# Optimization experiments

Hardware: AMD Instinct MI355X
Metric: run time of the kernel (lower is better)

Reference implementation:

```python
import jax, jax.numpy as jnp
import numpy as np

B, S, IN, H, NH = 64, 512, 512, 1024, 4
HD = H // NH
A, HID = 18, 1024
EPS = 1e-5


def _ln(x, w, eps=EPS):
    mu = jnp.mean(x, axis=-1, keepdims=True)
    var = jnp.mean((x - mu) ** 2, axis=-1, keepdims=True)
    return (x - mu) * jax.lax.rsqrt(var + eps) * w


def setup_inputs() -> dict:
    key = jax.random.key(0)
    ks = jax.random.split(key, 12)
    g = lambda k, shape, s: jax.random.normal(k, shape, jnp.float32) * s
    return {
        "obs": g(ks[0], (B, S, IN), 1.0),
        "slstm_state": jnp.zeros((4, B, H), jnp.float32),  # (y, c, n, m)
        "W_in": g(ks[1], (H, IN), IN ** -0.5),
        "b_in": jnp.zeros((H,), jnp.float32),
        "ln1_w": jnp.ones((H,), jnp.float32),
        "w_gates": g(ks[2], (4, NH, HD, HD), HD ** -0.5),  # i,f,z,o headwise input proj
        "R": g(ks[3], (NH, HD, 4, HD), HD ** -0.5),        # headwise recurrent kernel
        "b_gates": jnp.zeros((4, H), jnp.float32),
        "gn_w": jnp.ones((H,), jnp.float32),               # multi-head group norm weight
        "ln_post_w": jnp.ones((H,), jnp.float32),          # post-blocks norm
        "W_hid": g(ks[4], (HID, H), H ** -0.5), "b_hid": jnp.zeros((HID,), jnp.float32),
        "W_pol": g(ks[5], (HID, HID), HID ** -0.5), "b_pol": jnp.zeros((HID,), jnp.float32),
        "W_val": g(ks[6], (HID, HID), HID ** -0.5), "b_val": jnp.zeros((HID,), jnp.float32),
        "W_act": g(ks[7], (A, HID), 0.01), "b_act": jnp.zeros((A,), jnp.float32),
        "W_v": g(ks[8], (1, HID), HID ** -0.5), "b_v": jnp.zeros((1,), jnp.float32),
    }


def reference(obs, slstm_state, W_in, b_in, ln1_w, w_gates, R, b_gates, gn_w,
              ln_post_w, W_hid, b_hid, W_pol, b_pol, W_val, b_val, W_act, b_act, W_v, b_v):
    b, s, _ = obs.shape
    # input projection (input_size != hidden_size -> nn.Linear)
    x_proj = obs @ W_in.T + b_in                      # (B,S,H)
    # sLSTM block pre-norm
    xn = _ln(x_proj, ln1_w)
    xh = xn.reshape(b, s, NH, HD)
    # headwise (block-diagonal) gate input preactivations, time-major for scan
    gx = jnp.einsum('bsnd,gnde->sgbne', xh, w_gates)  # (S,4,B,NH,HD)
    bg = b_gates.reshape(4, 1, NH, HD)
    st = slstm_state.reshape(4, b, NH, HD)

    def step(carry, gx_t):
        h, c, n, m = carry
        raw = gx_t + jnp.einsum('bnd,ndge->gbne', h, R) + bg  # (4,B,NH,HD)
        iraw, fraw, zraw, oraw = raw
        logfplusm = m + jax.nn.log_sigmoid(fraw)
        mnew = jnp.maximum(iraw, logfplusm)
        i = jnp.exp(iraw - mnew)
        f = jnp.exp(logfplusm - mnew)
        cnew = f * c + i * jnp.tanh(zraw)
        nnew = f * n + i
        hnew = jax.nn.sigmoid(oraw) * cnew / nnew
        return (hnew, cnew, nnew, mnew), hnew

    _, ys = jax.lax.scan(step, (st[0], st[1], st[2], st[3]), gx)  # (S,B,NH,HD)
    y = jnp.transpose(ys, (1, 0, 2, 3))               # (B,S,NH,HD)
    # multi-head group norm over head_dim, then residual
    mu = jnp.mean(y, axis=-1, keepdims=True)
    var = jnp.mean((y - mu) ** 2, axis=-1, keepdims=True)
    y_gn = (y - mu) * jax.lax.rsqrt(var + EPS) * gn_w.reshape(NH, HD)
    out = x_proj + y_gn.reshape(b, s, H)
    out = _ln(out, ln_post_w)                         # post_blocks_norm
    # actor-critic heads
    hh = jax.nn.relu(out @ W_hid.T + b_hid)
    hp = jax.nn.relu(hh @ W_pol.T + b_pol)
    hv = jax.nn.relu(hh @ W_val.T + b_val)
    logits = hp @ W_act.T + b_act                     # (B,S,A)
    value = hv @ W_v.T + b_v                          # (B,S,1)
    return logits, value
```

## Files before the change

kernel.cpp:

```cpp
#include <hip/hip_runtime.h>
#include <cstdint>
#include <cstddef>

#define B_ 64
#define S_ 512
#define IN_ 512
#define H_ 1024
#define NH_ 4
#define HD_ 256
#define A_ 18
#define HID_ 1024
#define TCH_ 128
#define NCH_ (S_ / TCH_)

using short8 = __attribute__((ext_vector_type(8))) short;
using f32x4  = __attribute__((ext_vector_type(4))) float;

__device__ __forceinline__ unsigned short f2bf(float f) {
  union { float f; unsigned u; } c; c.f = f;
  unsigned r = c.u + 0x7FFFu + ((c.u >> 16) & 1u);
  return (unsigned short)(r >> 16);
}
__device__ __forceinline__ float bf2f(unsigned short h) {
  union { unsigned u; float f; } c; c.u = ((unsigned)h) << 16;
  return c.f;
}
__device__ __forceinline__ unsigned pk2(float a, float b) {
  return (unsigned)f2bf(a) | ((unsigned)f2bf(b) << 16);
}
__device__ __forceinline__ float dot2(unsigned a, unsigned b, float c) {
  float d;
  asm("v_dot2_f32_bf16 %0, %1, %2, %3" : "=v"(d) : "v"(a), "v"(b), "v"(c));
  return d;
}

__global__ __launch_bounds__(256) void rtrans_k(const float* __restrict__ R,
                                                unsigned* __restrict__ Rbb,
                                                unsigned* __restrict__ Rl) {
  const int i = blockIdx.x * 256 + threadIdx.x;
  const int dp = i & 127;
  const int e = (i >> 7) & 255;
  const int g = (i >> 15) & 3;
  const int nh = i >> 17;
  const float* rp = R + (((size_t)nh * 256 + 2 * dp) * 4 + g) * 256 + e;
  unsigned lo = f2bf(rp[0]), hi = f2bf(rp[1024]);
  unsigned v = lo | (hi << 16);
  Rbb[i] = v;
  if (dp >= 96) {
    int j = (dp - 96) >> 1, p = (dp - 96) & 1;
    int col = g * 256 + e;
    Rl[((size_t)(j * 4 + nh) * 1024 + col) * 2 + p] = v;
  }
}

__global__ __launch_bounds__(256) void wgt_k(const float* __restrict__ wg,
                                             unsigned short* __restrict__ wgb) {
  const int i = blockIdx.x * 256 + threadIdx.x;
  const int k = i & 255;
  const int e = (i >> 8) & 255;
  const int g = (i >> 16) & 3;
  const int nh = i >> 18;
  wgb[i] = f2bf(wg[(((size_t)(g * 4 + nh) * 256 + k) * 256) + e]);
}

__global__ __launch_bounds__(256) void wbf_k(const float* __restrict__ src,
                                             unsigned short* __restrict__ dst, int n) {
  int i = blockIdx.x * 256 + threadIdx.x;
  if (i < n) dst[i] = f2bf(src[i]);
}

__global__ __launch_bounds__(256) void rowstats_k(const unsigned short* __restrict__ x,
                                                  float* __restrict__ rs) {
  const int r = blockIdx.x, tid = threadIdx.x;
  const int lane = tid & 63, wave = tid >> 6;
  ushort4 u = *(const ushort4*)(x + (size_t)r * H_ + tid * 4);
  float v0 = bf2f(u.x), v1 = bf2f(u.y), v2 = bf2f(u.z), v3 = bf2f(u.w);
  float s1 = v0 + v1 + v2 + v3;
  float s2 = v0 * v0 + v1 * v1 + v2 * v2 + v3 * v3;
#pragma unroll
  for (int off = 32; off; off >>= 1) { s1 += __shfl_xor(s1, off); s2 += __shfl_xor(s2, off); }
  __shared__ float a1[4], a2[4];
  if (lane == 0) { a1[wave] = s1; a2[wave] = s2; }
  __syncthreads();
  if (tid == 0) {
    float S1 = a1[0] + a1[1] + a1[2] + a1[3];
    float S2 = a2[0] + a2[1] + a2[2] + a2[3];
    float mu = S1 * (1.f / H_);
    float var = S2 * (1.f / H_) - mu * mu;
    rs[r * 2] = mu;
    rs[r * 2 + 1] = rsqrtf(var + 1e-5f);
  }
}

template <int AMODE, int BMODE, bool RELU, int OUTMODE>
__global__ __launch_bounds__(256) void mgemm_k(
    const void* __restrict__ Av, const void* __restrict__ Wv,
    const float* __restrict__ bias, const float* __restrict__ rs,
    const float* __restrict__ lnw, unsigned short* __restrict__ Cb,
    int K, int lda, int chunk) {
  __shared__ uint4 As4[4][128];
  __shared__ uint4 Bs4[4][128];
  const int tid = threadIdx.x;
  const int lane = tid & 63, wave = tid >> 6;
  const int wr = wave >> 1, wc = wave & 1;
  const int col0 = blockIdx.y * 128;
  int nh = 0, g = 0, aoff = 0, bb = 0;
  size_t wbase = 0;
  if constexpr (OUTMODE == 1) {
    int z = blockIdx.z; nh = z >> 2; g = z & 3;
    aoff = nh * HD_;
    bb = blockIdx.x;
    wbase = (size_t)(nh * 4 + g) * 256 * 256;
  }
  auto arow = [&](int mm) -> int {
    if constexpr (OUTMODE == 1) return bb * 512 + chunk * TCH_ + mm;
    else return (int)blockIdx.x * 128 + mm;
  };
  f32x4 acc[4][4];
#pragma unroll
  for (int m = 0; m < 4; ++m)
#pragma unroll
    for (int n = 0; n < 4; ++n) acc[m][n] = 0.f;

  const int sm = tid >> 1;
  const int sh = tid & 1;

  for (int k0 = 0; k0 < K; k0 += 32) {
    {
      int rg = arow(sm);
      unsigned pk[8];
      if constexpr (AMODE == 0) {
        const float* ap = (const float*)Av + (size_t)rg * lda + k0 + sh * 16;
#pragma unroll
        for (int q = 0; q < 4; ++q) {
          float4 f = ((const float4*)ap)[q];
          pk[2 * q] = pk2(f.x, f.y); pk[2 * q + 1] = pk2(f.z, f.w);
        }
      } else if constexpr (AMODE == 1) {
        const uint4* ap = (const uint4*)((const unsigned short*)Av + (size_t)rg * lda + aoff + k0 + sh * 16);
        uint4 u0 = ap[0], u1 = ap[1];
        pk[0] = u0.x; pk[1] = u0.y; pk[2] = u0.z; pk[3] = u0.w;
        pk[4] = u1.x; pk[5] = u1.y; pk[6] = u1.z; pk[7] = u1.w;
      } else {
        const uint4* ap = (const uint4*)((const unsigned short*)Av + (size_t)rg * lda + aoff + k0 + sh * 16);
        uint4 u0 = ap[0], u1 = ap[1];
        unsigned w8[8] = {u0.x, u0.y, u0.z, u0.w, u1.x, u1.y, u1.z, u1.w};
        float mu = rs[rg * 2], rstd = rs[rg * 2 + 1];
        const float* lw = lnw + aoff + k0 + sh * 16;
#pragma unroll
        for (int q = 0; q < 8; ++q) {
          float lo = (bf2f((unsigned short)w8[q]) - mu) * rstd * lw[2 * q];
          float hi = (bf2f((unsigned short)(w8[q] >> 16)) - mu) * rstd * lw[2 * q + 1];
          pk[q] = pk2(lo, hi);
        }
      }
      As4[2 * sh][sm]     = uint4{pk[0], pk[1], pk[2], pk[3]};
      As4[2 * sh + 1][sm] = uint4{pk[4], pk[5], pk[6], pk[7]};
    }
    {
      unsigned pk[8];
      if constexpr (BMODE == 0) {
        const float* wp = (const float*)Wv + (size_t)(col0 + sm) * K + k0 + sh * 16;
#pragma unroll
        for (int q = 0; q < 4; ++q) {
          float4 f = ((const float4*)wp)[q];
          pk[2 * q] = pk2(f.x, f.y); pk[2 * q + 1] = pk2(f.z, f.w);
        }
      } else if constexpr (BMODE == 1) {
        const uint4* wp = (const uint4*)((const unsigned short*)Wv + wbase + (size_t)(col0 + sm) * 256 + k0 + sh * 16);
        uint4 u0 = wp[0], u1 = wp[1];
        pk[0] = u0.x; pk[1] = u0.y; pk[2] = u0.z; pk[3] = u0.w;
        pk[4] = u1.x; pk[5] = u1.y; pk[6] = u1.z; pk[7] = u1.w;
      } else {
        const uint4* wp = (const uint4*)((const unsigned short*)Wv + (size_t)(col0 + sm) * K + k0 + sh * 16);
        uint4 u0 = wp[0], u1 = wp[1];
        pk[0] = u0.x; pk[1] = u0.y; pk[2] = u0.z; pk[3] = u0.w;
        pk[4] = u1.x; pk[5] = u1.y; pk[6] = u1.z; pk[7] = u1.w;
      }
      Bs4[2 * sh][sm]     = uint4{pk[0], pk[1], pk[2], pk[3]};
      Bs4[2 * sh + 1][sm] = uint4{pk[4], pk[5], pk[6], pk[7]};
    }
    __syncthreads();
    short8 af[4], bfv[4];
#pragma unroll
    for (int m = 0; m < 4; ++m)
      af[m] = *(const short8*)&As4[lane >> 4][wr * 64 + m * 16 + (lane & 15)];
#pragma unroll
    for (int n = 0; n < 4; ++n)
      bfv[n] = *(const short8*)&Bs4[lane >> 4][wc * 64 + n * 16 + (lane & 15)];
#pragma unroll
    for (int m = 0; m < 4; ++m)
#pragma unroll
      for (int n = 0; n < 4; ++n)
        acc[m][n] = __builtin_amdgcn_mfma_f32_16x16x32_bf16(af[m], bfv[n], acc[m][n], 0, 0, 0);
    __syncthreads();
  }
  if constexpr (OUTMODE == 0) {
#pragma unroll
    for (int n = 0; n < 4; ++n) {
      int c = col0 + wc * 64 + n * 16 + (lane & 15);
      float bc = bias ? bias[c] : 0.f;
#pragma unroll
      for (int m = 0; m < 4; ++m) {
        int r0 = arow(wr * 64 + m * 16 + ((lane >> 4) << 2));
#pragma unroll
        for (int i = 0; i < 4; ++i) {
          float v = acc[m][n][i] + bc;
          if constexpr (RELU) v = fmaxf(v, 0.f);
          Cb[(size_t)(r0 + i) * 1024 + c] = f2bf(v);
        }
      }
    }
  } else {
#pragma unroll
    for (int n = 0; n < 4; ++n) {
      int e = col0 + wc * 64 + n * 16 + (lane & 15);
#pragma unroll
      for (int m = 0; m < 4; ++m) {
        int sl0 = wr * 64 + m * 16 + ((lane >> 4) << 2);
#pragma unroll
        for (int i = 0; i < 4; ++i) {
          int sl = sl0 + i;
          size_t base = (size_t)(sl * 64 + bb) * 4096 + nh * 1024 + g * 256;
          Cb[base + e] = f2bf(acc[m][n][i]);
        }
      }
    }
  }
}

__global__ __launch_bounds__(512, 2) void scan_k(
    const unsigned short* __restrict__ gxc, const unsigned* __restrict__ Rbb,
    const unsigned* __restrict__ Rl, const float* __restrict__ bgates,
    float* __restrict__ state, unsigned short* __restrict__ y, int chunk) {
  const int tid = threadIdx.x;
  const int bid = blockIdx.x;
  const int nh = bid >> 6, b = bid & 63;
  const int col0 = tid, col1 = tid + 512;
  const int g0 = col0 >> 8, g1 = col1 >> 8;
  __shared__ uint2 Rlds[16][1024];
  __shared__ float rawf[1024];
  __shared__ alignas(16) unsigned short hsu[256];

#pragma unroll
  for (int it = 0; it < 32; ++it) {
    int idx = it * 512 + tid;
    int j = idx >> 10, col = idx & 1023;
    Rlds[j][col] = ((const uint2*)Rl)[(size_t)(j * 4 + nh) * 1024 + col];
  }
  unsigned rc0[96], rc1[96];
  {
    const unsigned* rp0 = Rbb + ((size_t)nh * 1024 + col0) * 128;
    const unsigned* rp1 = Rbb + ((size_t)nh * 1024 + col1) * 128;
#pragma unroll
    for (int i = 0; i < 96; ++i) rc0[i] = rp0[i];
#pragma unroll
    for (int i = 0; i < 96; ++i) rc1[i] = rp1[i];
  }
  const float bg0 = bgates[g0 * H_ + nh * HD_ + (col0 & 255)];
  const float bg1 = bgates[g1 * H_ + nh * HD_ + (col1 & 255)];

  const size_t sbase = (size_t)b * H_ + nh * HD_ + tid;
  float c_ = 0.f, n_ = 0.f, m_ = 0.f, hlast = 0.f;
  if (tid < 256) {
    hlast = state[sbase];
    c_ = state[65536 + sbase];
    n_ = state[2 * 65536 + sbase];
    m_ = state[3 * 65536 + sbase];
    hsu[tid] = f2bf(hlast);
  }
  __syncthreads();

  const unsigned short* gp0 = gxc + ((size_t)b * 4 + nh) * 1024 + col0;
  const unsigned short* gp1 = gp0 + 512;
  unsigned short* yp = y + ((size_t)(chunk * TCH_) * 64 + b) * H_ + nh * HD_;

  unsigned short gc0 = gp0[0], gc1 = gp1[0];

  for (int t = 0; t < TCH_; ++t) {
    float acc0 = bf2f(gc0) + bg0;
    float acc1 = bf2f(gc1) + bg1;
    if (t < TCH_ - 1) {
      gc0 = gp0[(size_t)(t + 1) * 262144];
      gc1 = gp1[(size_t)(t + 1) * 262144];
    }
    const uint4* h4 = (const uint4*)hsu;
#pragma unroll
    for (int q = 0; q < 24; ++q) {
      uint4 hu = h4[q];
      acc0 = dot2(rc0[4 * q + 0], hu.x, acc0);
      acc1 = dot2(rc1[4 * q + 0], hu.x, acc1);
      acc0 = dot2(rc0[4 * q + 1], hu.y, acc0);
      acc1 = dot2(rc1[4 * q + 1], hu.y, acc1);
      acc0 = dot2(rc0[4 * q + 2], hu.z, acc0);
      acc1 = dot2(rc1[4 * q + 2], hu.z, acc1);
      acc0 = dot2(rc0[4 * q + 3], hu.w, acc0);
      acc1 = dot2(rc1[4 * q + 3], hu.w, acc1);
    }
#pragma unroll
    for (int s = 0; s < 8; ++s) {
      uint4 hu = h4[24 + s];
      uint2 a0 = Rlds[2 * s][col0];
      uint2 a1 = Rlds[2 * s + 1][col0];
      uint2 b0 = Rlds[2 * s][col1];
      uint2 b1 = Rlds[2 * s + 1][col1];
      acc0 = dot2(a0.x, hu.x, acc0);
      acc1 = dot2(b0.x, hu.x, acc1);
      acc0 = dot2(a0.y, hu.y, acc0);
      acc1 = dot2(b0.y, hu.y, acc1);
      acc0 = dot2(a1.x, hu.z, acc0);
      acc1 = dot2(b1.x, hu.z, acc1);
      acc0 = dot2(a1.y, hu.w, acc0);
      acc1 = dot2(b1.y, hu.w, acc1);
    }
    float val0, val1;
    if (g0 == 0) {
      val0 = acc0;
    } else {
      float ls = -log1pf(expf(-fabsf(acc0)));
      if (acc0 < 0.f) ls += acc0;
      val0 = ls;
    }
    if (g1 == 2) {
      val1 = tanhf(acc1);
    } else {
      val1 = 1.f / (1.f + expf(-acc1));
    }
    rawf[col0] = val0;
    rawf[col1] = val1;
    __syncthreads();
    if (tid < 256) {
      float iraw = rawf[tid];
      float ls   = rawf[256 + tid];
      float tz   = rawf[512 + tid];
      float sg   = rawf[768 + tid];
      float lfm = m_ + ls;
      float mnew = fmaxf(iraw, lfm);
      float iv = expf(iraw - mnew);
      float fv = expf(lfm - mnew);
      c_ = fv * c_ + iv * tz;
      n_ = fv * n_ + iv;
      m_ = mnew;
      hlast = sg * c_ / n_;
      unsigned short hb = f2bf(hlast);
      hsu[tid] = hb;
      yp[(size_t)t * 65536 + tid] = hb;
    }
    __syncthreads();
  }
  if (tid < 256) {
    state[sbase] = hlast;
    state[65536 + sbase] = c_;
    state[2 * 65536 + sbase] = n_;
    state[3 * 65536 + sbase] = m_;
  }
}

__global__ __launch_bounds__(256) void post_k(
    const unsigned short* __restrict__ y, const unsigned short* __restrict__ xp,
    const float* __restrict__ gnw, const float* __restrict__ lpw,
    unsigned short* __restrict__ outb) {
  const int r = blockIdx.x;
  const int b = r >> 9, s = r & 511;
  const int tid = threadIdx.x;
  const int lane = tid & 63, wave = tid >> 6;
  ushort4 yu = *(const ushort4*)(y + (size_t)(s * 64 + b) * H_ + tid * 4);
  float v[4] = {bf2f(yu.x), bf2f(yu.y), bf2f(yu.z), bf2f(yu.w)};
  float s1 = v[0] + v[1] + v[2] + v[3];
  float s2 = v[0] * v[0] + v[1] * v[1] + v[2] * v[2] + v[3] * v[3];
#pragma unroll
  for (int off = 32; off; off >>= 1) { s1 += __shfl_xor(s1, off); s2 += __shfl_xor(s2, off); }
  float mu = s1 * (1.f / HD_);
  float rstd = rsqrtf(s2 * (1.f / HD_) - mu * mu + 1e-5f);
  float4 g4 = *(const float4*)(gnw + tid * 4);
  ushort4 xu = *(const ushort4*)(xp + (size_t)r * H_ + tid * 4);
  float o[4];
  o[0] = fmaf((v[0] - mu) * rstd, g4.x, bf2f(xu.x));
  o[1] = fmaf((v[1] - mu) * rstd, g4.y, bf2f(xu.y));
  o[2] = fmaf((v[2] - mu) * rstd, g4.z, bf2f(xu.z));
  o[3] = fmaf((v[3] - mu) * rstd, g4.w, bf2f(xu.w));
  float t1 = o[0] + o[1] + o[2] + o[3];
  float t2 = o[0] * o[0] + o[1] * o[1] + o[2] * o[2] + o[3] * o[3];
#pragma unroll
  for (int off = 32; off; off >>= 1) { t1 += __shfl_xor(t1, off); t2 += __shfl_xor(t2, off); }
  __shared__ float a1[4], a2[4];
  if (lane == 0) { a1[wave] = t1; a2[wave] = t2; }
  __syncthreads();
  float T1 = a1[0] + a1[1] + a1[2] + a1[3];
  float T2 = a2[0] + a2[1] + a2[2] + a2[3];
  float MU = T1 * (1.f / H_);
  float RS = rsqrtf(T2 * (1.f / H_) - MU * MU + 1e-5f);
  float4 w4 = *(const float4*)(lpw + tid * 4);
  ushort4 res = {f2bf((o[0] - MU) * RS * w4.x), f2bf((o[1] - MU) * RS * w4.y),
                 f2bf((o[2] - MU) * RS * w4.z), f2bf((o[3] - MU) * RS * w4.w)};
  *(ushort4*)(outb + (size_t)r * H_ + tid * 4) = res;
}

__global__ __launch_bounds__(256) void heads_k(
    const unsigned short* __restrict__ hp, const unsigned short* __restrict__ hv,
    const float* __restrict__ Wact, const float* __restrict__ bact,
    const float* __restrict__ Wv, const float* __restrict__ bv,
    float* __restrict__ dout) {
  const int lane = threadIdx.x & 63, wave = threadIdx.x >> 6;
  const int r = blockIdx.x * 4 + wave;
  const unsigned short* hpr = hp + (size_t)r * HID_;
  const unsigned short* hvr = hv + (size_t)r * HID_;
  float acc[A_];
#pragma unroll
  for (int j = 0; j < A_; ++j) acc[j] = 0.f;
  float accv = 0.f;
  for (int i = 0; i < 16; ++i) {
    int k = i * 64 + lane;
    float hpv = bf2f(hpr[k]);
    float hvv = bf2f(hvr[k]);
#pragma unroll
    for (int j = 0; j < A_; ++j) acc[j] = fmaf(hpv, Wact[j * HID_ + k], acc[j]);
    accv = fmaf(hvv, Wv[k], accv);
  }
#pragma unroll
  for (int j = 0; j < A_; ++j)
#pragma unroll
    for (int off = 32; off; off >>= 1) acc[j] += __shfl_xor(acc[j], off);
#pragma unroll
  for (int off = 32; off; off >>= 1) accv += __shfl_xor(accv, off);
  if (lane == 0) {
#pragma unroll
    for (int j = 0; j < A_; ++j) dout[(size_t)r * A_ + j] = acc[j] + bact[j];
    dout[589824 + r] = accv + bv[0];
  }
}

extern "C" void kernel_launch(void* const* d_in, const int* in_sizes, int n_in,
                              void* d_out, int out_size, void* d_ws, size_t ws_size,
                              hipStream_t stream) {
  const float* obs   = (const float*)d_in[0];
  const float* st    = (const float*)d_in[1];
  const float* W_in  = (const float*)d_in[2];
  const float* b_in  = (const float*)d_in[3];
  const float* ln1w  = (const float*)d_in[4];
  const float* wg    = (const float*)d_in[5];
  const float* R     = (const float*)d_in[6];
  const float* bgat  = (const float*)d_in[7];
  const float* gnw   = (const float*)d_in[8];
  const float* lpw   = (const float*)d_in[9];
  const float* W_hid = (const float*)d_in[10];
  const float* b_hid = (const float*)d_in[11];
  const float* W_pol = (const float*)d_in[12];
  const float* b_pol = (const float*)d_in[13];
  const float* W_val = (const float*)d_in[14];
  const float* b_val = (const float*)d_in[15];
  const float* W_act = (const float*)d_in[16];
  const float* b_act = (const float*)d_in[17];
  const float* W_v   = (const float*)d_in[18];
  const float* b_v   = (const float*)d_in[19];

  const size_t NEEDED = 214958080;
  if (ws_size < NEEDED) return;
  char* ws = (char*)d_ws;
  unsigned short* xproj = (unsigned short*)(ws + 0);
  unsigned short* gxc   = (unsigned short*)(ws + 67108864);
  unsigned short* ybuf  = (unsigned short*)(ws + 134217728);
  float* statebuf       = (float*)(ws + 201326592);
  float* rstat          = (float*)(ws + 202375168);
  unsigned* Rbb         = (unsigned*)(ws + 202899456);
  unsigned short* wgb   = (unsigned short*)(ws + 204996608);
  unsigned* Rl          = (unsigned*)(ws + 207093760);
  unsigned short* wib   = (unsigned short*)(ws + 207618048);
  unsigned short* whb   = (unsigned short*)(ws + 208666624);
  unsigned short* wpb   = (unsigned short*)(ws + 210763776);
  unsigned short* wvb   = (unsigned short*)(ws + 212860928);
  unsigned short* outb  = gxc;
  unsigned short* hh    = xproj;
  unsigned short* hp    = ybuf;
  unsigned short* hv    = gxc;
  float* dout = (float*)d_out;

  hipMemcpyAsync(statebuf, st, 4 * 65536 * sizeof(float), hipMemcpyDeviceToDevice, stream);
  rtrans_k<<<2048, 256, 0, stream>>>(R, Rbb, Rl);
  wgt_k<<<4096, 256, 0, stream>>>(wg, wgb);
  wbf_k<<<2048, 256, 0, stream>>>(W_in, wib, 524288);
  wbf_k<<<4096, 256, 0, stream>>>(W_hid, whb, 1048576);
  wbf_k<<<4096, 256, 0, stream>>>(W_pol, wpb, 1048576);
  wbf_k<<<4096, 256, 0, stream>>>(W_val, wvb, 1048576);
  mgemm_k<0, 2, false, 0><<<dim3(256, 8), 256, 0, stream>>>(
      obs, wib, b_in, nullptr, nullptr, xproj, 512, 512, 0);
  rowstats_k<<<32768, 256, 0, stream>>>(xproj, rstat);
  for (int c = 0; c < NCH_; ++c) {
    mgemm_k<2, 1, false, 1><<<dim3(64, 2, 16), 256, 0, stream>>>(
        xproj, wgb, nullptr, rstat, ln1w, gxc, 256, 1024, c);
    scan_k<<<256, 512, 0, stream>>>(gxc, Rbb, Rl, bgat, statebuf, ybuf, c);
  }
  post_k<<<32768, 256, 0, stream>>>(ybuf, xproj, gnw, lpw, outb);
  mgemm_k<1, 2, true, 0><<<dim3(256, 8), 256, 0, stream>>>(
      outb, whb, b_hid, nullptr, nullptr, hh, 1024, 1024, 0);
  mgemm_k<1, 2, true, 0><<<dim3(256, 8), 256, 0, stream>>>(
      hh, wpb, b_pol, nullptr, nullptr, hp, 1024, 1024, 0);
  mgemm_k<1, 2, true, 0><<<dim3(256, 8), 256, 0, stream>>>(
      hh, wvb, b_val, nullptr, nullptr, hv, 1024, 1024, 0);
  heads_k<<<8192, 256, 0, stream>>>(hp, hv, W_act, b_act, W_v, b_v, dout);
}
```

Baseline: 2.067 ms.

## Broadcast recurrent state via readlane SGPRs and widen LDS R-tile loads

In the recurrent scan, each lane now loads one 16-byte slice of the hidden state, and the values are broadcast with readlane into scalar registers that feed v_dot2 directly. This replaces the per-iteration LDS broadcast reads of h. The LDS-resident part of R is relaid out (and the prep kernel rewritten to match) so each column reads one uint4 per step instead of two uint2. Each column's dot product is split into two accumulators to shorten the dependency chain. The cost is extra readlane instructions and a slight change in floating-point summation order.

Measured after the change: 2.012 ms. 2.7% less time.

```diff
diff --git a/kernel.cpp b/kernel.cpp
--- a/kernel.cpp
+++ b/kernel.cpp
@@ -28,9 +28,9 @@
 __device__ __forceinline__ unsigned pk2(float a, float b) {
   return (unsigned)f2bf(a) | ((unsigned)f2bf(b) << 16);
 }
-__device__ __forceinline__ float dot2(unsigned a, unsigned b, float c) {
+__device__ __forceinline__ float dot2s(unsigned r, unsigned h_sgpr, float c) {
   float d;
-  asm("v_dot2_f32_bf16 %0, %1, %2, %3" : "=v"(d) : "v"(a), "v"(b), "v"(c));
+  asm("v_dot2_f32_bf16 %0, %1, %2, %3" : "=v"(d) : "v"(r), "s"(h_sgpr), "v"(c));
   return d;
 }
 
@@ -47,9 +47,9 @@
   unsigned v = lo | (hi << 16);
   Rbb[i] = v;
   if (dp >= 96) {
-    int j = (dp - 96) >> 1, p = (dp - 96) & 1;
+    int s = (dp - 96) >> 2, j = (dp - 96) & 3;
     int col = g * 256 + e;
-    Rl[((size_t)(j * 4 + nh) * 1024 + col) * 2 + p] = v;
+    Rl[((size_t)(nh * 1024 + col) * 8 + s) * 4 + j] = v;
   }
 }
 
@@ -234,19 +234,19 @@
     const unsigned* __restrict__ Rl, const float* __restrict__ bgates,
     float* __restrict__ state, unsigned short* __restrict__ y, int chunk) {
   const int tid = threadIdx.x;
+  const int lane = tid & 63;
   const int bid = blockIdx.x;
   const int nh = bid >> 6, b = bid & 63;
   const int col0 = tid, col1 = tid + 512;
   const int g0 = col0 >> 8, g1 = col1 >> 8;
-  __shared__ uint2 Rlds[16][1024];
+  __shared__ uint4 Rlds4[8][1024];
   __shared__ float rawf[1024];
   __shared__ alignas(16) unsigned short hsu[256];
 
 #pragma unroll
-  for (int it = 0; it < 32; ++it) {
+  for (int it = 0; it < 16; ++it) {
     int idx = it * 512 + tid;
-    int j = idx >> 10, col = idx & 1023;
-    Rlds[j][col] = ((const uint2*)Rl)[(size_t)(j * 4 + nh) * 1024 + col];
+    Rlds4[idx & 7][idx >> 3] = ((const uint4*)Rl)[(size_t)nh * 8192 + idx];
   }
   unsigned rc0[96], rc1[96];
   {
@@ -278,41 +278,48 @@
   unsigned short gc0 = gp0[0], gc1 = gp1[0];
 
   for (int t = 0; t < TCH_; ++t) {
-    float acc0 = bf2f(gc0) + bg0;
-    float acc1 = bf2f(gc1) + bg1;
+    float a0a = bf2f(gc0) + bg0, a0b = 0.f;
+    float a1a = bf2f(gc1) + bg1, a1b = 0.f;
     if (t < TCH_ - 1) {
       gc0 = gp0[(size_t)(t + 1) * 262144];
       gc1 = gp1[(size_t)(t + 1) * 262144];
     }
-    const uint4* h4 = (const uint4*)hsu;
+    uint4 hc = ((const uint4*)hsu)[lane & 31];
 #pragma unroll
     for (int q = 0; q < 24; ++q) {
-      uint4 hu = h4[q];
-      acc0 = dot2(rc0[4 * q + 0], hu.x, acc0);
-      acc1 = dot2(rc1[4 * q + 0], hu.x, acc1);
-      acc0 = dot2(rc0[4 * q + 1], hu.y, acc0);
-      acc1 = dot2(rc1[4 * q + 1], hu.y, acc1);
-      acc0 = dot2(rc0[4 * q + 2], hu.z, acc0);
-      acc1 = dot2(rc1[4 * q + 2], hu.z, acc1);
-      acc0 = dot2(rc0[4 * q + 3], hu.w, acc0);
-      acc1 = dot2(rc1[4 * q + 3], hu.w, acc1);
+      unsigned h0 = __builtin_amdgcn_readlane(hc.x, q);
+      unsigned h1 = __builtin_amdgcn_readlane(hc.y, q);
+      unsigned h2 = __builtin_amdgcn_readlane(hc.z, q);
+      unsigned h3 = __builtin_amdgcn_readlane(hc.w, q);
+      a0a = dot2s(rc0[4 * q + 0], h0, a0a);
+      a1a = dot2s(rc1[4 * q + 0], h0, a1a);
+      a0a = dot2s(rc0[4 * q + 1], h1, a0a);
+      a1a = dot2s(rc1[4 * q + 1], h1, a1a);
+      a0b = dot2s(rc0[4 * q + 2], h2, a0b);
+      a1b = dot2s(rc1[4 * q + 2], h2, a1b);
+      a0b = dot2s(rc0[4 * q + 3], h3, a0b);
+      a1b = dot2s(rc1[4 * q + 3], h3, a1b);
     }
 #pragma unroll
     for (int s = 0; s < 8; ++s) {
-      uint4 hu = h4[24 + s];
-      uint2 a0 = Rlds[2 * s][col0];
-      uint2 a1 = Rlds[2 * s + 1][col0];
-      uint2 b0 = Rlds[2 * s][col1];
-      uint2 b1 = Rlds[2 * s + 1][col1];
-      acc0 = dot2(a0.x, hu.x, acc0);
-      acc1 = dot2(b0.x, hu.x, acc1);
-      acc0 = dot2(a0.y, hu.y, acc0);
-      acc1 = dot2(b0.y, hu.y, acc1);
-      acc0 = dot2(a1.x, hu.z, acc0);
-      acc1 = dot2(b1.x, hu.z, acc1);
-      acc0 = dot2(a1.y, hu.w, acc0);
-      acc1 = dot2(b1.y, hu.w, acc1);
-    }
+      int q = 24 + s;
+      unsigned h0 = __builtin_amdgcn_readlane(hc.x, q);
+      unsigned h1 = __builtin_amdgcn_readlane(hc.y, q);
+      unsigned h2 = __builtin_amdgcn_readlane(hc.z, q);
+      unsigned h3 = __builtin_amdgcn_readlane(hc.w, q);
+      uint4 ra = Rlds4[s][col0];
+      uint4 rb = Rlds4[s][col1];
+      a0a = dot2s(ra.x, h0, a0a);
+      a1a = dot2s(rb.x, h0, a1a);
+      a0a = dot2s(ra.y, h1, a0a);
+      a1a = dot2s(rb.y, h1, a1a);
+      a0b = dot2s(ra.z, h2, a0b);
+      a1b = dot2s(rb.z, h2, a1b);
+      a0b = dot2s(ra.w, h3, a0b);
+      a1b = dot2s(rb.w, h3, a1b);
+    }
+    float acc0 = a0a + a0b;
+    float acc1 = a1a + a1b;
     float val0, val1;
     if (g0 == 0) {
       val0 = acc0;
```
